# Optimization experiments

Hardware: AMD Instinct MI355X
Metric: run time of the kernel (lower is better)

Reference implementation:

```python
import jax, jax.numpy as jnp
import numpy as np
from jax import lax

D_STATE = 16
D_CONV = 4
EPS = 1e-6


def setup_inputs() -> dict:
    key = jax.random.key(0)
    ks = jax.random.split(key, 8)
    B, L, H = 2, 2048, 1024
    d_inner = 2 * H
    s = lambda n: 1.0 / np.sqrt(n)
    x = jax.random.normal(ks[0], (B, L, H), jnp.float32)
    norm_w = jnp.ones((H,), jnp.float32)
    w_in = jax.random.normal(ks[1], (H, 2 * d_inner), jnp.float32) * s(H)
    conv_w = jax.random.normal(ks[2], (d_inner, 1, D_CONV), jnp.float32) * s(D_CONV)
    conv_b = jnp.zeros((d_inner,), jnp.float32)
    w_xproj = jax.random.normal(ks[3], (d_inner, 2 * D_STATE + d_inner), jnp.float32) * s(d_inner)
    # A_log as in torch init: log(arange(1..d_state)) broadcast over d_inner
    A_log = jnp.broadcast_to(jnp.log(jnp.arange(1, D_STATE + 1, dtype=jnp.float32)), (d_inner, D_STATE))
    D_param = jnp.ones((d_inner,), jnp.float32)
    w_out = jax.random.normal(ks[4], (d_inner, H), jnp.float32) * s(d_inner)
    return {"x": x, "norm_w": norm_w, "w_in": w_in, "conv_w": conv_w,
            "conv_b": conv_b, "w_xproj": w_xproj, "A_log": A_log,
            "D_param": D_param, "w_out": w_out}


def _rmsnorm(x, w):
    var = jnp.mean(x * x, axis=-1, keepdims=True)
    return x * lax.rsqrt(var + EPS) * w


def _silu(x):
    return x * jax.nn.sigmoid(x)


def _mamba_forward(x, norm_w, w_in, conv_w, conv_b, w_xproj, A_log, D_param, w_out):
    B, L, H = x.shape
    d_inner = w_in.shape[1] // 2
    residual = x
    h = _rmsnorm(x, norm_w)
    xz = h @ w_in                               # [B, L, 2*d_inner]
    x_ssm, z = jnp.split(xz, 2, axis=-1)
    # causal depthwise conv1d (torch pads both sides then slices -> causal left pad)
    xc = jnp.swapaxes(x_ssm, 1, 2)              # [B, d_inner, L]
    xc = jnp.pad(xc, ((0, 0), (0, 0), (D_CONV - 1, 0)))
    xc = lax.conv_general_dilated(xc, conv_w, (1,), 'VALID',
                                  feature_group_count=d_inner)
    xc = xc + conv_b[None, :, None]
    x_ssm = _silu(jnp.swapaxes(xc, 1, 2))       # [B, L, d_inner]
    proj = x_ssm @ w_xproj
    B_in = proj[..., :D_STATE]                  # [B, L, n]
    C_in = proj[..., D_STATE:2 * D_STATE]
    delta = jax.nn.softplus(proj[..., 2 * D_STATE:])  # [B, L, d_inner]
    A = -jnp.exp(A_log)                         # [d_inner, n]

    def step(hst, inp):
        xs, dt, Bt, Ct = inp                    # [B,d], [B,d], [B,n], [B,n]
        dA = jnp.exp(dt[..., None] * A)         # [B, d, n]
        hst = dA * hst + (dt * xs)[..., None] * Bt[:, None, :]
        y = jnp.einsum('bdn,bn->bd', hst, Ct)
        return hst, y

    h0 = jnp.zeros((B, d_inner, D_STATE), x_ssm.dtype)
    xs_t = jnp.swapaxes(x_ssm, 0, 1)            # [L, B, d]
    dt_t = jnp.swapaxes(delta, 0, 1)
    Bt_t = jnp.swapaxes(B_in, 0, 1)
    Ct_t = jnp.swapaxes(C_in, 0, 1)
    _, ys = lax.scan(step, h0, (xs_t, dt_t, Bt_t, Ct_t))
    y = jnp.swapaxes(ys, 0, 1)                  # [B, L, d]
    y = (y + D_param * x_ssm) * _silu(z)
    return residual + y @ w_out


def reference(x, norm_w, w_in, conv_w, conv_b, w_xproj, A_log, D_param, w_out):
    return _mamba_forward(x, norm_w, w_in, conv_w, conv_b, w_xproj, A_log, D_param, w_out)
```

## Files before the change

### kernel.cpp

```cpp
#include <hip/hip_runtime.h>
#include <math.h>

#define BATCH 2
#define LSEQ  2048
#define HDIM  1024
#define DI    2048
#define DS    16
#define NPROJ 2080
#define TOK   4096
#define NCH   64
#define CLEN  32

typedef _Float16 f16;
typedef _Float16 f16x8 __attribute__((ext_vector_type(8)));
typedef _Float16 f16x4 __attribute__((ext_vector_type(4)));
typedef float    f32x4 __attribute__((ext_vector_type(4)));

__device__ __forceinline__ float siluf(float v) { return v / (1.f + __expf(-v)); }
__device__ __forceinline__ float softplusf(float v) {
  return v > 20.f ? v : log1pf(__expf(v));
}

__device__ __forceinline__ void gload16(const void* g, void* l) {
  __builtin_amdgcn_global_load_lds(
      (const __attribute__((address_space(1))) void*)g,
      (__attribute__((address_space(3))) void*)l, 16, 0, 0);
}

__global__ __launch_bounds__(256) void k_transpose(
    const float* __restrict__ W, f16* __restrict__ Wt, int R, int C) {
  __shared__ float t[32][33];
  int c0 = blockIdx.x * 32, r0 = blockIdx.y * 32;
  int tx = threadIdx.x & 31, ty = threadIdx.x >> 5;
#pragma unroll
  for (int i = 0; i < 4; ++i) {
    int r = ty + i * 8;
    t[r][tx] = W[(size_t)(r0 + r) * C + c0 + tx];
  }
  __syncthreads();
#pragma unroll
  for (int i = 0; i < 4; ++i) {
    int r = ty + i * 8;
    Wt[(size_t)(c0 + r) * R + r0 + tx] = (f16)t[tx][r];
  }
}

__global__ __launch_bounds__(256) void k_rmsnorm(
    const float* __restrict__ x, const float* __restrict__ w, f16* __restrict__ h) {
  int t = blockIdx.x;
  int tid = threadIdx.x;
  float4 v = reinterpret_cast<const float4*>(x + (size_t)t * HDIM)[tid];
  float ss = v.x * v.x + v.y * v.y + v.z * v.z + v.w * v.w;
#pragma unroll
  for (int off = 32; off; off >>= 1) ss += __shfl_down(ss, off, 64);
  __shared__ float sred[4];
  if ((tid & 63) == 0) sred[tid >> 6] = ss;
  __syncthreads();
  float tot = sred[0] + sred[1] + sred[2] + sred[3];
  float scale = rsqrtf(tot * (1.f / HDIM) + 1e-6f);
  float4 wv = reinterpret_cast<const float4*>(w)[tid];
  f16x4 o;
  o[0] = (f16)(v.x * scale * wv.x);
  o[1] = (f16)(v.y * scale * wv.y);
  o[2] = (f16)(v.z * scale * wv.z);
  o[3] = (f16)(v.w * scale * wv.w);
  *reinterpret_cast<f16x4*>(h + (size_t)t * HDIM + tid * 4) = o;
}

template <int MODE>
__global__ __launch_bounds__(256) void k_mgemm(
    const f16* __restrict__ A, const f16* __restrict__ Bt,
    float* __restrict__ C, const float* __restrict__ R,
    f16* __restrict__ Ox, f16* __restrict__ Oz,
    int M, int N, int K) {
  __shared__ __align__(16) f16 At[2 * 128 * 32];
  __shared__ __align__(16) f16 Bs[2 * 128 * 32];
  const int tid = threadIdx.x;
  const int lane = tid & 63;
  const int w = tid >> 6;
  const int wm = w >> 1, wn = w & 1;

  const int gx = gridDim.x;
  const int nwg = gx * gridDim.y;
  const int bid = blockIdx.y * gx + blockIdx.x;
  const int q = nwg >> 3, r = nwg & 7;
  const int xcd = bid & 7, idx = bid >> 3;
  const int swzb = (xcd < r ? xcd * (q + 1) : r * (q + 1) + (xcd - r) * q) + idx;
  const int m0 = (swzb / gx) * 128, n0 = (swzb % gx) * 128;
  const int Nlim = N - 1;

  const int ls = lane >> 2;
  const int kq = lane & 3;
  const int rowA0 = w * 16 + ls;
  const int rowA1 = rowA0 + 64;
  const int swz = ((kq << 4) ^ ((rowA0 & 3) << 4)) >> 1;
  const f16* gA0 = A + (size_t)(m0 + rowA0) * K + swz;
  const f16* gA1 = A + (size_t)(m0 + rowA1) * K + swz;
  int rb0 = n0 + rowA0; rb0 = rb0 > Nlim ? Nlim : rb0;
  int rb1 = n0 + rowA1; rb1 = rb1 > Nlim ? Nlim : rb1;
  const f16* gB0 = Bt + (size_t)rb0 * K + swz;
  const f16* gB1 = Bt + (size_t)rb1 * K + swz;
  const int ld0 = w * 1024 + (lane << 4);
  const int ld1 = (w + 4) * 1024 + (lane << 4);

  const int fr = lane & 15;
  const int kgb = (lane >> 4) << 4;
  int offA[4], offB[4];
#pragma unroll
  for (int i = 0; i < 4; ++i) {
    int ra = wm * 64 + i * 16 + fr;
    offA[i] = ra * 64 + (kgb ^ ((ra & 3) << 4));
    int rbx = wn * 64 + i * 16 + fr;
    offB[i] = rbx * 64 + (kgb ^ ((rbx & 3) << 4));
  }

  f32x4 acc[4][4];
#pragma unroll
  for (int i = 0; i < 4; ++i)
#pragma unroll
    for (int j = 0; j < 4; ++j) acc[i][j] = (f32x4){0.f, 0.f, 0.f, 0.f};

  const int nt = K >> 5;

#define STAGE(buf, tt)                                                   \
  {                                                                      \
    const int ke = (tt) << 5;                                            \
    gload16(gA0 + ke, (char*)At + (buf)*8192 + ld0);                     \
    gload16(gA1 + ke, (char*)At + (buf)*8192 + ld1);                     \
    gload16(gB0 + ke, (char*)Bs + (buf)*8192 + ld0);                     \
    gload16(gB1 + ke, (char*)Bs + (buf)*8192 + ld1);                     \
  }

#define COMPUTE(buf)                                                     \
  {                                                                      \
    const char* bA = (const char*)At + (buf)*8192;                       \
    const char* bB = (const char*)Bs + (buf)*8192;                       \
    f16x8 a[4], b[4];                                                    \
    _Pragma("unroll") for (int mi = 0; mi < 4; ++mi)                     \
        a[mi] = *(const f16x8*)(bA + offA[mi]);                          \
    _Pragma("unroll") for (int ni = 0; ni < 4; ++ni)                     \
        b[ni] = *(const f16x8*)(bB + offB[ni]);                          \
    _Pragma("unroll") for (int mi = 0; mi < 4; ++mi)                     \
        _Pragma("unroll") for (int ni = 0; ni < 4; ++ni)                 \
            acc[mi][ni] = __builtin_amdgcn_mfma_f32_16x16x32_f16(        \
                a[mi], b[ni], acc[mi][ni], 0, 0, 0);                     \
  }

  STAGE(0, 0);
  asm volatile("s_waitcnt vmcnt(0)" ::: "memory");
  __builtin_amdgcn_s_barrier();

  for (int t = 0; t < nt; t += 2) {
    if (t + 1 < nt) STAGE(1, t + 1);
    COMPUTE(0);
    asm volatile("s_waitcnt vmcnt(0)" ::: "memory");
    __builtin_amdgcn_s_barrier();
    if (t + 2 < nt) STAGE(0, t + 2);
    COMPUTE(1);
    asm volatile("s_waitcnt vmcnt(0)" ::: "memory");
    __builtin_amdgcn_s_barrier();
  }
#undef STAGE
#undef COMPUTE

  const int r4 = (lane >> 4) << 2;
#pragma unroll
  for (int mi = 0; mi < 4; ++mi) {
#pragma unroll
    for (int ni = 0; ni < 4; ++ni) {
      int col = n0 + wn * 64 + ni * 16 + fr;
      if (col < N) {
        int mrow = m0 + wm * 64 + mi * 16 + r4;
#pragma unroll
        for (int j = 0; j < 4; ++j) {
          float v = acc[mi][ni][j];
          if (MODE == 1) {
            if (col >= 2 * DS) v = softplusf(v);
            C[(size_t)(mrow + j) * N + col] = v;
          } else if (MODE == 2) {
            size_t o = (size_t)(mrow + j) * N + col;
            C[o] = v + R[o];
          } else {
            if (col < DI) Ox[(size_t)(mrow + j) * DI + col] = (f16)v;
            else          Oz[(size_t)(mrow + j) * DI + col - DI] = (f16)v;
          }
        }
      }
    }
  }
}

__global__ __launch_bounds__(256) void k_conv(
    const f16* __restrict__ xr, const float* __restrict__ cw,
    const float* __restrict__ cb, f16* __restrict__ xs) {
  size_t idx = (size_t)blockIdx.x * 256 + threadIdx.x;
  int d = (int)(idx & (DI - 1));
  size_t tf = idx >> 11;
  int t = (int)(tf & (LSEQ - 1));
  const f16* base = xr + tf * DI + d;
  float acc = cb[d];
  float w0 = cw[d * 4 + 0], w1 = cw[d * 4 + 1], w2 = cw[d * 4 + 2], w3 = cw[d * 4 + 3];
  acc = fmaf(w3, (float)base[0], acc);
  if (t >= 1) acc = fmaf(w2, (float)base[-(ptrdiff_t)DI], acc);
  if (t >= 2) acc = fmaf(w1, (float)base[-(ptrdiff_t)(2 * DI)], acc);
  if (t >= 3) acc = fmaf(w0, (float)base[-(ptrdiff_t)(3 * DI)], acc);
  xs[idx] = (f16)siluf(acc);
}


__global__ __launch_bounds__(256) void k_scanA(
    const float* __restrict__ proj, const f16* __restrict__ xs,
    const float* __restrict__ A_log,
    float* __restrict__ Atot, float* __restrict__ Hend) {
  int gid = blockIdx.x * 256 + threadIdx.x;
  int d = gid & (DI - 1);
  int b = (gid >> 11) & (BATCH - 1);
  int c = gid >> 12;
  float Ad[DS];
  {
    const float4* ap = reinterpret_cast<const float4*>(A_log + (size_t)d * DS);
#pragma unroll
    for (int i = 0; i < 4; ++i) {
      float4 v = ap[i];
      Ad[4 * i + 0] = -__expf(v.x);
      Ad[4 * i + 1] = -__expf(v.y);
      Ad[4 * i + 2] = -__expf(v.z);
      Ad[4 * i + 3] = -__expf(v.w);
    }
  }
  float h[DS], P[DS];
#pragma unroll
  for (int n = 0; n < DS; ++n) { h[n] = 0.f; P[n] = 1.f; }
  const float* prow = proj + ((size_t)b * LSEQ + (size_t)c * CLEN) * NPROJ;
  const f16* xrow = xs + ((size_t)b * LSEQ + (size_t)c * CLEN) * DI + d;
  for (int t = 0; t < CLEN; ++t) {
    const float* pr = prow + (size_t)t * NPROJ;
    float dt = pr[2 * DS + d];
    float xv = (float)xrow[(size_t)t * DI];
    float Bv[DS];
    {
      const float4* p4 = reinterpret_cast<const float4*>(pr);
#pragma unroll
      for (int i = 0; i < 4; ++i) {
        float4 v = p4[i];
        Bv[4 * i + 0] = v.x; Bv[4 * i + 1] = v.y;
        Bv[4 * i + 2] = v.z; Bv[4 * i + 3] = v.w;
      }
    }
    float dxv = dt * xv;
#pragma unroll
    for (int n = 0; n < DS; ++n) {
      float da = __expf(dt * Ad[n]);
      P[n] *= da;
      h[n] = fmaf(da, h[n], dxv * Bv[n]);
    }
  }
  float4* ao = reinterpret_cast<float4*>(Atot + (size_t)gid * DS);
  float4* ho = reinterpret_cast<float4*>(Hend + (size_t)gid * DS);
#pragma unroll
  for (int i = 0; i < 4; ++i) {
    ao[i] = make_float4(P[4 * i], P[4 * i + 1], P[4 * i + 2], P[4 * i + 3]);
    ho[i] = make_float4(h[4 * i], h[4 * i + 1], h[4 * i + 2], h[4 * i + 3]);
  }
}

__global__ __launch_bounds__(256) void k_scanB(
    float* __restrict__ Atot, const float* __restrict__ Hend) {
  int gid = blockIdx.x * 256 + threadIdx.x;
  float h = 0.f;
#pragma unroll
  for (int c = 0; c < NCH; ++c) {
    size_t idx = (size_t)c * (BATCH * DI * DS) + gid;
    float P = Atot[idx];
    Atot[idx] = h;
    h = fmaf(P, h, Hend[idx]);
  }
}

__global__ __launch_bounds__(256) void k_scanC(
    const float* __restrict__ proj, const f16* __restrict__ xs,
    const f16* __restrict__ z16, const float* __restrict__ A_log,
    const float* __restrict__ Dp, const float* __restrict__ Hin,
    f16* __restrict__ yg) {
  int gid = blockIdx.x * 256 + threadIdx.x;
  int d = gid & (DI - 1);
  int b = (gid >> 11) & (BATCH - 1);
  int c = gid >> 12;
  float Ad[DS];
  {
    const float4* ap = reinterpret_cast<const float4*>(A_log + (size_t)d * DS);
#pragma unroll
    for (int i = 0; i < 4; ++i) {
      float4 v = ap[i];
      Ad[4 * i + 0] = -__expf(v.x);
      Ad[4 * i + 1] = -__expf(v.y);
      Ad[4 * i + 2] = -__expf(v.z);
      Ad[4 * i + 3] = -__expf(v.w);
    }
  }
  float h[DS];
  {
    const float4* hi = reinterpret_cast<const float4*>(Hin + (size_t)gid * DS);
#pragma unroll
    for (int i = 0; i < 4; ++i) {
      float4 v = hi[i];
      h[4 * i + 0] = v.x; h[4 * i + 1] = v.y;
      h[4 * i + 2] = v.z; h[4 * i + 3] = v.w;
    }
  }
  float Dd = Dp[d];
  const float* prow = proj + ((size_t)b * LSEQ + (size_t)c * CLEN) * NPROJ;
  const f16* xrow = xs + ((size_t)b * LSEQ + (size_t)c * CLEN) * DI + d;
  const f16* zrow = z16 + ((size_t)b * LSEQ + (size_t)c * CLEN) * DI + d;
  f16* yrow = yg + ((size_t)b * LSEQ + (size_t)c * CLEN) * DI + d;
  for (int t = 0; t < CLEN; ++t) {
    const float* pr = prow + (size_t)t * NPROJ;
    float dt = pr[2 * DS + d];
    float xv = (float)xrow[(size_t)t * DI];
    float Bv[DS], Cv[DS];
    {
      const float4* p4 = reinterpret_cast<const float4*>(pr);
#pragma unroll
      for (int i = 0; i < 4; ++i) {
        float4 v = p4[i];
        Bv[4 * i + 0] = v.x; Bv[4 * i + 1] = v.y;
        Bv[4 * i + 2] = v.z; Bv[4 * i + 3] = v.w;
      }
#pragma unroll
      for (int i = 0; i < 4; ++i) {
        float4 v = p4[4 + i];
        Cv[4 * i + 0] = v.x; Cv[4 * i + 1] = v.y;
        Cv[4 * i + 2] = v.z; Cv[4 * i + 3] = v.w;
      }
    }
    float dxv = dt * xv;
    float y = 0.f;
#pragma unroll
    for (int n = 0; n < DS; ++n) {
      float da = __expf(dt * Ad[n]);
      h[n] = fmaf(da, h[n], dxv * Bv[n]);
      y = fmaf(h[n], Cv[n], y);
    }
    float z = (float)zrow[(size_t)t * DI];
    yrow[(size_t)t * DI] = (f16)((y + Dd * xv) * siluf(z));
  }
}

extern "C" void kernel_launch(void* const* d_in, const int* in_sizes, int n_in,
                              void* d_out, int out_size, void* d_ws, size_t ws_size,
                              hipStream_t stream) {
  const float* x       = (const float*)d_in[0];
  const float* norm_w  = (const float*)d_in[1];
  const float* w_in    = (const float*)d_in[2];
  const float* conv_w  = (const float*)d_in[3];
  const float* conv_b  = (const float*)d_in[4];
  const float* w_xproj = (const float*)d_in[5];
  const float* A_log   = (const float*)d_in[6];
  const float* D_param = (const float*)d_in[7];
  const float* w_out   = (const float*)d_in[8];
  float* out = (float*)d_out;

  char* ws = (char*)d_ws;
  size_t off = 0;
  float* proj  = (float*)(ws + off); off += (size_t)TOK * NPROJ * 4;
  f16*   xr16  = (f16*)(ws + off);   off += (size_t)TOK * DI * 2;
  f16*   z16   = (f16*)(ws + off);   off += (size_t)TOK * DI * 2;
  f16*   h16   = (f16*)(ws + off);   off += (size_t)TOK * HDIM * 2;
  f16*   xs16  = (f16*)(ws + off);   off += (size_t)TOK * DI * 2;
  f16*   yg16  = (f16*)(ws + off);   off += (size_t)TOK * DI * 2;
  f16*   winT  = (f16*)(ws + off);   off += (size_t)2 * DI * HDIM * 2;
  f16*   wxT   = (f16*)(ws + off);   off += (size_t)NPROJ * DI * 2;
  f16*   woT   = (f16*)(ws + off);   off += (size_t)HDIM * DI * 2;
  const size_t SCN = (size_t)NCH * BATCH * DI * DS;
  float* Atot  = (float*)(ws + off); off += SCN * 4;
  float* Hend  = (float*)(ws + off); off += SCN * 4;

  k_transpose<<<dim3((2 * DI) / 32, HDIM / 32), 256, 0, stream>>>(w_in, winT, HDIM, 2 * DI);
  k_transpose<<<dim3(NPROJ / 32, DI / 32), 256, 0, stream>>>(w_xproj, wxT, DI, NPROJ);
  k_transpose<<<dim3(HDIM / 32, DI / 32), 256, 0, stream>>>(w_out, woT, DI, HDIM);
  k_rmsnorm<<<TOK, 256, 0, stream>>>(x, norm_w, h16);
  k_mgemm<3><<<dim3((2 * DI) / 128, TOK / 128), 256, 0, stream>>>(
      h16, winT, nullptr, nullptr, xr16, z16, TOK, 2 * DI, HDIM);
  k_conv<<<(TOK * DI) / 256, 256, 0, stream>>>(xr16, conv_w, conv_b, xs16);
  k_mgemm<1><<<dim3(17, TOK / 128), 256, 0, stream>>>(
      xs16, wxT, proj, nullptr, nullptr, nullptr, TOK, NPROJ, DI);
  const int NTH = NCH * BATCH * DI;
  k_scanA<<<NTH / 256, 256, 0, stream>>>(proj, xs16, A_log, Atot, Hend);
  k_scanB<<<(BATCH * DI * DS) / 256, 256, 0, stream>>>(Atot, Hend);
  k_scanC<<<NTH / 256, 256, 0, stream>>>(proj, xs16, z16, A_log, D_param,
                                         Atot, yg16);
  k_mgemm<2><<<dim3(HDIM / 128, TOK / 128), 256, 0, stream>>>(
      yg16, woT, out, x, nullptr, nullptr, TOK, HDIM, DI);
}
```

Before: 465.9 us.

## Parameterize GEMM M-tile and drop LDS double-buffering for single-stage loop

Templates the GEMM on the M-tile height so the x-projection and output GEMMs use 64-row tiles, doubling their workgroup counts to fill more CUs. It also removes the two-stage LDS double-buffer pipeline and uses a single buffer with syncthreads around each K-step. The smaller tiles are meant to raise occupancy and improve load balance. In exchange they lower data reuse, and the removed prefetch overlap exposes global-load latency on every iteration, including in the large input GEMM.

```diff
diff --git a/kernel.cpp b/kernel.cpp
--- a/kernel.cpp
+++ b/kernel.cpp
@@ -67,14 +67,16 @@
   *reinterpret_cast<f16x4*>(h + (size_t)t * HDIM + tid * 4) = o;
 }
 
-template <int MODE>
+template <int MODE, int MI>
 __global__ __launch_bounds__(256) void k_mgemm(
     const f16* __restrict__ A, const f16* __restrict__ Bt,
     float* __restrict__ C, const float* __restrict__ R,
     f16* __restrict__ Ox, f16* __restrict__ Oz,
     int M, int N, int K) {
-  __shared__ __align__(16) f16 At[2 * 128 * 32];
-  __shared__ __align__(16) f16 Bs[2 * 128 * 32];
+  constexpr int BM = MI * 32;
+  constexpr int NA = MI / 2;
+  __shared__ __align__(16) f16 At[BM * 32];
+  __shared__ __align__(16) f16 Bs[128 * 32];
   const int tid = threadIdx.x;
   const int lane = tid & 63;
   const int w = tid >> 6;
@@ -84,93 +86,86 @@
   const int nwg = gx * gridDim.y;
   const int bid = blockIdx.y * gx + blockIdx.x;
   const int q = nwg >> 3, r = nwg & 7;
-  const int xcd = bid & 7, idx = bid >> 3;
-  const int swzb = (xcd < r ? xcd * (q + 1) : r * (q + 1) + (xcd - r) * q) + idx;
-  const int m0 = (swzb / gx) * 128, n0 = (swzb % gx) * 128;
+  const int xcd = bid & 7, ix = bid >> 3;
+  const int swzb = (xcd < r ? xcd * (q + 1) : r * (q + 1) + (xcd - r) * q) + ix;
+  const int m0 = (swzb / gx) * BM, n0 = (swzb % gx) * 128;
   const int Nlim = N - 1;
 
   const int ls = lane >> 2;
   const int kq = lane & 3;
-  const int rowA0 = w * 16 + ls;
-  const int rowA1 = rowA0 + 64;
-  const int swz = ((kq << 4) ^ ((rowA0 & 3) << 4)) >> 1;
-  const f16* gA0 = A + (size_t)(m0 + rowA0) * K + swz;
-  const f16* gA1 = A + (size_t)(m0 + rowA1) * K + swz;
-  int rb0 = n0 + rowA0; rb0 = rb0 > Nlim ? Nlim : rb0;
-  int rb1 = n0 + rowA1; rb1 = rb1 > Nlim ? Nlim : rb1;
-  const f16* gB0 = Bt + (size_t)rb0 * K + swz;
-  const f16* gB1 = Bt + (size_t)rb1 * K + swz;
-  const int ld0 = w * 1024 + (lane << 4);
-  const int ld1 = (w + 4) * 1024 + (lane << 4);
+  const int lofs = lane << 4;
+  const f16* gA[NA];
+  int ldA[NA];
+#pragma unroll
+  for (int i = 0; i < NA; ++i) {
+    int c = w + i * 4;
+    int row = c * 16 + ls;
+    int swz = ((kq << 4) ^ ((row & 3) << 4)) >> 1;
+    gA[i] = A + (size_t)(m0 + row) * K + swz;
+    ldA[i] = c * 1024 + lofs;
+  }
+  const f16* gB[2];
+  int ldB[2];
+#pragma unroll
+  for (int i = 0; i < 2; ++i) {
+    int c = w + i * 4;
+    int row = c * 16 + ls;
+    int swz = ((kq << 4) ^ ((row & 3) << 4)) >> 1;
+    int rb = n0 + row; rb = rb > Nlim ? Nlim : rb;
+    gB[i] = Bt + (size_t)rb * K + swz;
+    ldB[i] = c * 1024 + lofs;
+  }
 
   const int fr = lane & 15;
   const int kgb = (lane >> 4) << 4;
-  int offA[4], offB[4];
+  int offA[MI], offB[4];
+#pragma unroll
+  for (int i = 0; i < MI; ++i) {
+    int ra = wm * (MI * 16) + i * 16 + fr;
+    offA[i] = ra * 64 + (kgb ^ ((ra & 3) << 4));
+  }
 #pragma unroll
   for (int i = 0; i < 4; ++i) {
-    int ra = wm * 64 + i * 16 + fr;
-    offA[i] = ra * 64 + (kgb ^ ((ra & 3) << 4));
-    int rbx = wn * 64 + i * 16 + fr;
-    offB[i] = rbx * 64 + (kgb ^ ((rbx & 3) << 4));
-  }
-
-  f32x4 acc[4][4];
-#pragma unroll
-  for (int i = 0; i < 4; ++i)
+    int rbw = wn * 64 + i * 16 + fr;
+    offB[i] = rbw * 64 + (kgb ^ ((rbw & 3) << 4));
+  }
+
+  f32x4 acc[MI][4];
+#pragma unroll
+  for (int i = 0; i < MI; ++i)
 #pragma unroll
     for (int j = 0; j < 4; ++j) acc[i][j] = (f32x4){0.f, 0.f, 0.f, 0.f};
 
   const int nt = K >> 5;
-
-#define STAGE(buf, tt)                                                   \
-  {                                                                      \
-    const int ke = (tt) << 5;                                            \
-    gload16(gA0 + ke, (char*)At + (buf)*8192 + ld0);                     \
-    gload16(gA1 + ke, (char*)At + (buf)*8192 + ld1);                     \
-    gload16(gB0 + ke, (char*)Bs + (buf)*8192 + ld0);                     \
-    gload16(gB1 + ke, (char*)Bs + (buf)*8192 + ld1);                     \
-  }
-
-#define COMPUTE(buf)                                                     \
-  {                                                                      \
-    const char* bA = (const char*)At + (buf)*8192;                       \
-    const char* bB = (const char*)Bs + (buf)*8192;                       \
-    f16x8 a[4], b[4];                                                    \
-    _Pragma("unroll") for (int mi = 0; mi < 4; ++mi)                     \
-        a[mi] = *(const f16x8*)(bA + offA[mi]);                          \
-    _Pragma("unroll") for (int ni = 0; ni < 4; ++ni)                     \
-        b[ni] = *(const f16x8*)(bB + offB[ni]);                          \
-    _Pragma("unroll") for (int mi = 0; mi < 4; ++mi)                     \
-        _Pragma("unroll") for (int ni = 0; ni < 4; ++ni)                 \
-            acc[mi][ni] = __builtin_amdgcn_mfma_f32_16x16x32_f16(        \
-                a[mi], b[ni], acc[mi][ni], 0, 0, 0);                     \
-  }
-
-  STAGE(0, 0);
-  asm volatile("s_waitcnt vmcnt(0)" ::: "memory");
-  __builtin_amdgcn_s_barrier();
-
-  for (int t = 0; t < nt; t += 2) {
-    if (t + 1 < nt) STAGE(1, t + 1);
-    COMPUTE(0);
-    asm volatile("s_waitcnt vmcnt(0)" ::: "memory");
-    __builtin_amdgcn_s_barrier();
-    if (t + 2 < nt) STAGE(0, t + 2);
-    COMPUTE(1);
-    asm volatile("s_waitcnt vmcnt(0)" ::: "memory");
-    __builtin_amdgcn_s_barrier();
-  }
-#undef STAGE
-#undef COMPUTE
+  for (int t = 0; t < nt; ++t) {
+    const int ke = t << 5;
+#pragma unroll
+    for (int i = 0; i < NA; ++i) gload16(gA[i] + ke, (char*)At + ldA[i]);
+#pragma unroll
+    for (int i = 0; i < 2; ++i) gload16(gB[i] + ke, (char*)Bs + ldB[i]);
+    __syncthreads();
+    f16x8 a[MI], b[4];
+#pragma unroll
+    for (int mi = 0; mi < MI; ++mi) a[mi] = *(const f16x8*)((char*)At + offA[mi]);
+#pragma unroll
+    for (int ni = 0; ni < 4; ++ni) b[ni] = *(const f16x8*)((char*)Bs + offB[ni]);
+#pragma unroll
+    for (int mi = 0; mi < MI; ++mi)
+#pragma unroll
+      for (int ni = 0; ni < 4; ++ni)
+        acc[mi][ni] = __builtin_amdgcn_mfma_f32_16x16x32_f16(
+            a[mi], b[ni], acc[mi][ni], 0, 0, 0);
+    __syncthreads();
+  }
 
   const int r4 = (lane >> 4) << 2;
 #pragma unroll
-  for (int mi = 0; mi < 4; ++mi) {
+  for (int mi = 0; mi < MI; ++mi) {
 #pragma unroll
     for (int ni = 0; ni < 4; ++ni) {
       int col = n0 + wn * 64 + ni * 16 + fr;
       if (col < N) {
-        int mrow = m0 + wm * 64 + mi * 16 + r4;
+        int mrow = m0 + wm * (MI * 16) + mi * 16 + r4;
 #pragma unroll
         for (int j = 0; j < 4; ++j) {
           float v = acc[mi][ni][j];
@@ -379,16 +374,16 @@
   k_transpose<<<dim3(NPROJ / 32, DI / 32), 256, 0, stream>>>(w_xproj, wxT, DI, NPROJ);
   k_transpose<<<dim3(HDIM / 32, DI / 32), 256, 0, stream>>>(w_out, woT, DI, HDIM);
   k_rmsnorm<<<TOK, 256, 0, stream>>>(x, norm_w, h16);
-  k_mgemm<3><<<dim3((2 * DI) / 128, TOK / 128), 256, 0, stream>>>(
+  k_mgemm<3, 4><<<dim3((2 * DI) / 128, TOK / 128), 256, 0, stream>>>(
       h16, winT, nullptr, nullptr, xr16, z16, TOK, 2 * DI, HDIM);
   k_conv<<<(TOK * DI) / 256, 256, 0, stream>>>(xr16, conv_w, conv_b, xs16);
-  k_mgemm<1><<<dim3(17, TOK / 128), 256, 0, stream>>>(
+  k_mgemm<1, 2><<<dim3(17, TOK / 64), 256, 0, stream>>>(
       xs16, wxT, proj, nullptr, nullptr, nullptr, TOK, NPROJ, DI);
   const int NTH = NCH * BATCH * DI;
   k_scanA<<<NTH / 256, 256, 0, stream>>>(proj, xs16, A_log, Atot, Hend);
   k_scanB<<<(BATCH * DI * DS) / 256, 256, 0, stream>>>(Atot, Hend);
   k_scanC<<<NTH / 256, 256, 0, stream>>>(proj, xs16, z16, A_log, D_param,
                                          Atot, yg16);
-  k_mgemm<2><<<dim3(HDIM / 128, TOK / 128), 256, 0, stream>>>(
+  k_mgemm<2, 2><<<dim3(HDIM / 128, TOK / 64), 256, 0, stream>>>(
       yg16, woT, out, x, nullptr, nullptr, TOK, HDIM, DI);
 }
```

Measured after the change: 440.4 us. 5.5% less time.
